# Performance work log

Hardware: AMD Instinct MI355X
Metric: run time of the kernel (lower is better)

The kernel has to match this reference:

```python
import jax, jax.numpy as jnp
import numpy as np

B, H = 1024, 256
HP = H // 2  # hyperparams_dim
W_SCALE = 0.08  # kaiming-uniform-like magnitude to keep tanh unsaturated


def setup_inputs() -> dict:
    key = jax.random.key(0)
    ks = jax.random.split(key, 8)
    return {
        "h_0": jax.random.normal(ks[0], (B, 1, H), dtype=jnp.float32),
        "h_t": jax.random.normal(ks[1], (B, 1, H), dtype=jnp.float32),
        "msg": jax.random.normal(ks[2], (B, 1, H), dtype=jnp.float32),
        "c": jax.random.uniform(ks[3], (1,), dtype=jnp.float32),
        "fc1_w": jax.random.normal(ks[4], (HP, H), dtype=jnp.float32) * W_SCALE,
        "fc2_w": jax.random.normal(ks[5], (HP, HP), dtype=jnp.float32) * W_SCALE,
        "fc3_w": jax.random.normal(ks[6], (HP, HP), dtype=jnp.float32) * W_SCALE,
        "fc4_w": jax.random.normal(ks[7], (2 * H * H, HP), dtype=jnp.float32) * W_SCALE,
    }


def reference(h_0, h_t, msg, c, fc1_w, fc2_w, fc3_w, fc4_w):
    # torch code clamps self.c into [0, 1] before use
    cc = jnp.clip(c, 0.0, 1.0)
    h = cc * h_0 + (1.0 - cc) * h_t                     # [B, 1, H]
    x = jnp.tanh(jnp.einsum('bsh,ph->bsp', h, fc1_w))    # [B, 1, HP]
    x = jnp.tanh(jnp.einsum('bsp,qp->bsq', x, fc2_w))    # [B, 1, HP]
    x = jnp.tanh(jnp.einsum('bsq,rq->bsr', x, fc3_w))    # [B, 1, HP]
    f4 = jnp.einsum('bsr,wr->bsw', x, fc4_w)             # [B, 1, 2*H*H]
    g1 = f4[..., : H * H].reshape(-1, H, H)              # [B, H, H]
    g2 = f4[..., H * H :].reshape(-1, H, H)              # [B, H, H]
    # F.linear(msg[i], g) == msg[i] @ g.T, batched over B
    g1_out = jnp.tanh(jnp.einsum('bsh,bkh->bsk', msg, g1))  # [B, 1, H]
    out = jnp.einsum('bsk,bok->bso', g1_out, g2)             # [B, 1, H]
    return out
```

## Files before the change

### kernel.cpp

```cpp
#include <hip/hip_runtime.h>
#include <hip/hip_bf16.h>

#define HDIM 256
#define HPDIM 128

typedef short bf8 __attribute__((ext_vector_type(8)));
typedef float f32x4 __attribute__((ext_vector_type(4)));

__device__ inline unsigned pkbf2(float a, float b) {
  float2 f; f.x = a; f.y = b;
  __hip_bfloat162 h = __float22bfloat162_rn(f);
  unsigned u; __builtin_memcpy(&u, &h, 4); return u;
}
__device__ inline unsigned short bfbits(float v) {
  __hip_bfloat16 h = __float2bfloat16(v);
  unsigned short u; __builtin_memcpy(&u, &h, 2); return u;
}
__device__ inline uint4 pack8u(float4 a, float4 b) {
  uint4 r;
  r.x = pkbf2(a.x, a.y); r.y = pkbf2(a.z, a.w);
  r.z = pkbf2(b.x, b.y); r.w = pkbf2(b.z, b.w);
  return r;
}
__device__ inline float fast_tanh(float x) {
  float t = __expf(2.0f * x);
  return 1.0f - 2.0f * __builtin_amdgcn_rcpf(t + 1.0f);
}
__device__ inline bf8 wfrag(const float* __restrict__ s) {
  float4 a = *(const float4*)s, b = *(const float4*)(s + 4);
  uint4 u = pack8u(a, b);
  bf8 r; __builtin_memcpy(&r, &u, 16); return r;
}

typedef const __attribute__((address_space(1))) unsigned int* gas_ptr;
typedef __attribute__((address_space(3))) unsigned int* las_ptr;
__device__ inline void gld_lds16(const void* g, void* l) {
  __builtin_amdgcn_global_load_lds((gas_ptr)g, (las_ptr)l, 16, 0, 0);
}

__global__ __launch_bounds__(256) void k_prep(
    const float* __restrict__ h0, const float* __restrict__ htv,
    const float* __restrict__ cp,
    const float* __restrict__ w1, const float* __restrict__ w2,
    const float* __restrict__ w3, const float* __restrict__ msg,
    short* __restrict__ x3f, float* __restrict__ msgTT) {
  const int t = threadIdx.x;
  const int bx = blockIdx.x;

  if (bx >= 64) {
    const int b0 = (bx - 64) * 64;
    #pragma unroll
    for (int it = 0; it < 16; ++it) {
      int u = it * 256 + t;
      int bl = u & 63, g = u >> 6;
      float4 v = *(const float4*)(msg + (size_t)(b0 + bl) * HDIM + g * 4);
      *(float4*)(msgTT + (size_t)g * 4096 + (b0 + bl) * 4) = v;
    }
    return;
  }

  __shared__ char hbuf[8192];
  __shared__ char xa[4096];
  __shared__ char xb[4096];
  const int wave = t >> 6, lane = t & 63;
  const int r16 = lane & 15, quad = lane >> 4;
  const int b0 = bx * 16;
  const float cc = fminf(fmaxf(cp[0], 0.f), 1.f);

  #pragma unroll
  for (int it = 0; it < 2; ++it) {
    int flat = it * 2048 + t * 8;
    int row = flat >> 8, col = flat & 255, kb = col >> 3;
    int gi = (b0 + row) * HDIM + col;
    float4 a = *(const float4*)(h0 + gi);
    float4 b = *(const float4*)(htv + gi);
    float4 va, vb;
    va.x = cc*a.x + (1.f-cc)*b.x; va.y = cc*a.y + (1.f-cc)*b.y;
    va.z = cc*a.z + (1.f-cc)*b.z; va.w = cc*a.w + (1.f-cc)*b.w;
    a = *(const float4*)(h0 + gi + 4); b = *(const float4*)(htv + gi + 4);
    vb.x = cc*a.x + (1.f-cc)*b.x; vb.y = cc*a.y + (1.f-cc)*b.y;
    vb.z = cc*a.z + (1.f-cc)*b.z; vb.w = cc*a.w + (1.f-cc)*b.w;
    *(uint4*)(hbuf + row*512 + ((kb ^ (row & 7)) << 4)) = pack8u(va, vb);
  }
  __syncthreads();

  {
    f32x4 acc[2] = {};
    #pragma unroll
    for (int ks = 0; ks < 8; ++ks) {
      bf8 af = *(bf8*)(hbuf + r16*512 + (((ks*4 + quad) ^ (r16 & 7)) << 4));
      #pragma unroll
      for (int nt = 0; nt < 2; ++nt) {
        bf8 bw_ = wfrag(w1 + ((wave*2 + nt)*16 + r16) * 256 + ks*32 + quad*8);
        acc[nt] = __builtin_amdgcn_mfma_f32_16x16x32_bf16(af, bw_, acc[nt], 0, 0, 0);
      }
    }
    #pragma unroll
    for (int nt = 0; nt < 2; ++nt)
      #pragma unroll
      for (int i = 0; i < 4; ++i) {
        int row = quad*4 + i, col = wave*32 + nt*16 + r16;
        *(unsigned short*)(xa + row*256 + (((col >> 3) ^ (row & 7)) << 4) + ((col & 7) << 1))
            = bfbits(fast_tanh(acc[nt][i]));
      }
  }
  __syncthreads();
  {
    f32x4 acc[2] = {};
    #pragma unroll
    for (int ks = 0; ks < 4; ++ks) {
      bf8 af = *(bf8*)(xa + r16*256 + (((ks*4 + quad) ^ (r16 & 7)) << 4));
      #pragma unroll
      for (int nt = 0; nt < 2; ++nt) {
        bf8 bw_ = wfrag(w2 + ((wave*2 + nt)*16 + r16) * 128 + ks*32 + quad*8);
        acc[nt] = __builtin_amdgcn_mfma_f32_16x16x32_bf16(af, bw_, acc[nt], 0, 0, 0);
      }
    }
    #pragma unroll
    for (int nt = 0; nt < 2; ++nt)
      #pragma unroll
      for (int i = 0; i < 4; ++i) {
        int row = quad*4 + i, col = wave*32 + nt*16 + r16;
        *(unsigned short*)(xb + row*256 + (((col >> 3) ^ (row & 7)) << 4) + ((col & 7) << 1))
            = bfbits(fast_tanh(acc[nt][i]));
      }
  }
  __syncthreads();
  {
    f32x4 acc[2] = {};
    #pragma unroll
    for (int ks = 0; ks < 4; ++ks) {
      bf8 af = *(bf8*)(xb + r16*256 + (((ks*4 + quad) ^ (r16 & 7)) << 4));
      #pragma unroll
      for (int nt = 0; nt < 2; ++nt) {
        bf8 bw_ = wfrag(w3 + ((wave*2 + nt)*16 + r16) * 128 + ks*32 + quad*8);
        acc[nt] = __builtin_amdgcn_mfma_f32_16x16x32_bf16(af, bw_, acc[nt], 0, 0, 0);
      }
    }
    #pragma unroll
    for (int nt = 0; nt < 2; ++nt)
      #pragma unroll
      for (int i = 0; i < 4; ++i) {
        int row = quad*4 + i, col = wave*32 + nt*16 + r16;
        *(unsigned short*)(xa + row*256 + (((col >> 3) ^ (row & 7)) << 4) + ((col & 7) << 1))
            = bfbits(fast_tanh(acc[nt][i]));
      }
  }
  __syncthreads();
  {
    int ks = t >> 6, l = t & 63, q2 = l >> 4, rr = l & 15;
    uint4 d = *(uint4*)(xa + rr*256 + (((ks*4 + q2) ^ (rr & 7)) << 4));
    *(uint4*)(x3f + (size_t)((bx*4 + ks)*64 + l)*8) = d;
  }
}

template<int PHASE>
__global__ __launch_bounds__(1024, 4) void k_hyper(
    const short* __restrict__ x3f, const float* __restrict__ wTT,
    const float* __restrict__ fc4, float* __restrict__ outp) {
  __shared__ char lds[65536 + 49152];
  char* slab = lds;
  char* ring = lds + 65536;
  const int bxs = blockIdx.x;
  const int kcol = ((bxs & 7) << 5) | (bxs >> 3);
  const int t = threadIdx.x, wave = t >> 6, lane = t & 63;
  const int r16 = lane & 15, quad = lane >> 4;
  const int bw = wave * 64;

  const float* src = fc4 + ((size_t)(PHASE ? 65536 : 0) + (size_t)kcol * 256) * HPDIM;

  gld_lds16(src + t * 4, ring + t * 16);

  bf8 xf[4][4];
  #pragma unroll
  for (int nt = 0; nt < 4; ++nt)
    #pragma unroll
    for (int ks = 0; ks < 4; ++ks)
      xf[nt][ks] = *(const bf8*)(x3f +
          (size_t)(((wave*4 + nt)*4 + ks)*64 + lane)*8);
  #pragma unroll
  for (int nt = 0; nt < 4; ++nt)
    #pragma unroll
    for (int ks = 0; ks < 4; ++ks)
      asm volatile("" : "+v"(xf[nt][ks]));

  #pragma unroll
  for (int c = 0; c < 8; ++c) {
    if (c < 7)
      gld_lds16(src + (c + 1) * 4096 + t * 4, ring + ((c + 1) % 3) * 16384 + t * 16);
    if (c < 7) asm volatile("s_waitcnt vmcnt(1) lgkmcnt(0)" ::: "memory");
    else       asm volatile("s_waitcnt vmcnt(0) lgkmcnt(0)" ::: "memory");
    __builtin_amdgcn_s_barrier();
    __builtin_amdgcn_sched_barrier(0);
    {
      f32x4 v = *(const f32x4*)(ring + (c % 3) * 16384 + t * 16);
      int row = c * 32 + (t >> 5), kb = (t & 31) >> 1;
      uint2 o; o.x = pkbf2(v[0], v[1]); o.y = pkbf2(v[2], v[3]);
      *(uint2*)(slab + row * 256 + ((kb ^ (row & 7)) << 4) + (t & 1) * 8) = o;
    }
  }
  __syncthreads();

  float gacc[4] = {0.f, 0.f, 0.f, 0.f};
  const float* wbase = wTT + (size_t)quad * 4096 + (bw + r16) * 4;

  #pragma unroll 1
  for (int hg = 0; hg < 16; ++hg) {
    float4 wv[4];
    #pragma unroll
    for (int nt = 0; nt < 4; ++nt)
      wv[nt] = *(const float4*)(wbase + (size_t)hg*16384 + nt*64);
    const int row = hg*16 + r16;
    bf8 af[4];
    #pragma unroll
    for (int ks = 0; ks < 4; ++ks)
      af[ks] = *(bf8*)(slab + row*256 + (((ks*4 + quad) ^ (row & 7)) << 4));
    #pragma unroll
    for (int nt = 0; nt < 4; ++nt) {
      f32x4 acc = {};
      #pragma unroll
      for (int ks = 0; ks < 4; ++ks)
        acc = __builtin_amdgcn_mfma_f32_16x16x32_bf16(af[ks], xf[nt][ks], acc, 0, 0, 0);
      gacc[nt] += acc[0]*wv[nt].x + acc[1]*wv[nt].y + acc[2]*wv[nt].z + acc[3]*wv[nt].w;
    }
  }

  #pragma unroll
  for (int nt = 0; nt < 4; ++nt) {
    float v = gacc[nt];
    v += __shfl_xor(v, 16);
    v += __shfl_xor(v, 32);
    if (quad == 0) {
      int b = bw + nt*16 + r16;
      if (PHASE == 0) outp[(size_t)(kcol >> 2)*4096 + b*4 + (kcol & 3)] = fast_tanh(v);
      else            outp[b*HDIM + kcol] = v;
    }
  }
}

extern "C" void kernel_launch(void* const* d_in, const int* in_sizes, int n_in,
                              void* d_out, int out_size, void* d_ws, size_t ws_size,
                              hipStream_t stream) {
  const float* h0  = (const float*)d_in[0];
  const float* htt = (const float*)d_in[1];
  const float* msg = (const float*)d_in[2];
  const float* c   = (const float*)d_in[3];
  const float* w1  = (const float*)d_in[4];
  const float* w2  = (const float*)d_in[5];
  const float* w3  = (const float*)d_in[6];
  const float* w4  = (const float*)d_in[7];
  float* out = (float*)d_out;

  short* x3f  = (short*)d_ws;
  float* g1TT = (float*)((char*)d_ws + 262144);
  float* msgTT= (float*)((char*)d_ws + 262144 + 1048576);

  k_prep<<<dim3(80), dim3(256), 0, stream>>>(h0, htt, c, w1, w2, w3, msg,
                                             x3f, msgTT);
  k_hyper<0><<<dim3(256), dim3(1024), 0, stream>>>(x3f, msgTT, w4, g1TT);
  k_hyper<1><<<dim3(256), dim3(1024), 0, stream>>>(x3f, g1TT, w4, out);
}
```

Measured before the change: 155.6 us.

## Overlap fc4 chunk streaming with MFMA compute using a double-buffered ring

New measurement: 215.2 us. 38.3% more time.

```diff
diff --git a/kernel.cpp b/kernel.cpp
--- a/kernel.cpp
+++ b/kernel.cpp
@@ -158,7 +158,7 @@
 __global__ __launch_bounds__(1024, 4) void k_hyper(
     const short* __restrict__ x3f, const float* __restrict__ wTT,
     const float* __restrict__ fc4, float* __restrict__ outp) {
-  __shared__ char lds[65536 + 49152];
+  __shared__ char lds[65536 + 32768];
   char* slab = lds;
   char* ring = lds + 65536;
   const int bxs = blockIdx.x;
@@ -184,44 +184,61 @@
     for (int ks = 0; ks < 4; ++ks)
       asm volatile("" : "+v"(xf[nt][ks]));
 
-  #pragma unroll
-  for (int c = 0; c < 8; ++c) {
-    if (c < 7)
-      gld_lds16(src + (c + 1) * 4096 + t * 4, ring + ((c + 1) % 3) * 16384 + t * 16);
-    if (c < 7) asm volatile("s_waitcnt vmcnt(1) lgkmcnt(0)" ::: "memory");
-    else       asm volatile("s_waitcnt vmcnt(0) lgkmcnt(0)" ::: "memory");
-    __builtin_amdgcn_s_barrier();
-    __builtin_amdgcn_sched_barrier(0);
-    {
-      f32x4 v = *(const f32x4*)(ring + (c % 3) * 16384 + t * 16);
-      int row = c * 32 + (t >> 5), kb = (t & 31) >> 1;
-      uint2 o; o.x = pkbf2(v[0], v[1]); o.y = pkbf2(v[2], v[3]);
-      *(uint2*)(slab + row * 256 + ((kb ^ (row & 7)) << 4) + (t & 1) * 8) = o;
-    }
-  }
-  __syncthreads();
+  asm volatile("s_waitcnt vmcnt(0) lgkmcnt(0)" ::: "memory");
+  __builtin_amdgcn_sched_barrier(0);
+  __builtin_amdgcn_s_barrier();
+  {
+    f32x4 v = *(const f32x4*)(ring + t * 16);
+    int row = t >> 5, kb = (t & 31) >> 1;
+    uint2 o; o.x = pkbf2(v[0], v[1]); o.y = pkbf2(v[2], v[3]);
+    *(uint2*)(slab + row * 256 + ((kb ^ (row & 7)) << 4) + (t & 1) * 8) = o;
+  }
+  gld_lds16(src + 4096 + t * 4, ring + 16384 + t * 16);
+  asm volatile("s_waitcnt lgkmcnt(0)" ::: "memory");
+  __builtin_amdgcn_sched_barrier(0);
+  __builtin_amdgcn_s_barrier();
 
   float gacc[4] = {0.f, 0.f, 0.f, 0.f};
   const float* wbase = wTT + (size_t)quad * 4096 + (bw + r16) * 4;
 
   #pragma unroll 1
-  for (int hg = 0; hg < 16; ++hg) {
-    float4 wv[4];
-    #pragma unroll
-    for (int nt = 0; nt < 4; ++nt)
-      wv[nt] = *(const float4*)(wbase + (size_t)hg*16384 + nt*64);
-    const int row = hg*16 + r16;
-    bf8 af[4];
-    #pragma unroll
-    for (int ks = 0; ks < 4; ++ks)
-      af[ks] = *(bf8*)(slab + row*256 + (((ks*4 + quad) ^ (row & 7)) << 4));
-    #pragma unroll
-    for (int nt = 0; nt < 4; ++nt) {
-      f32x4 acc = {};
+  for (int c = 0; c < 8; ++c) {
+    #pragma unroll
+    for (int hh = 0; hh < 2; ++hh) {
+      const int hg = c * 2 + hh;
+      float4 wv[4];
+      #pragma unroll
+      for (int nt = 0; nt < 4; ++nt)
+        wv[nt] = *(const float4*)(wbase + (size_t)hg*16384 + nt*64);
+      const int row = hg*16 + r16;
+      bf8 af[4];
       #pragma unroll
       for (int ks = 0; ks < 4; ++ks)
-        acc = __builtin_amdgcn_mfma_f32_16x16x32_bf16(af[ks], xf[nt][ks], acc, 0, 0, 0);
-      gacc[nt] += acc[0]*wv[nt].x + acc[1]*wv[nt].y + acc[2]*wv[nt].z + acc[3]*wv[nt].w;
+        af[ks] = *(bf8*)(slab + row*256 + (((ks*4 + quad) ^ (row & 7)) << 4));
+      #pragma unroll
+      for (int nt = 0; nt < 4; ++nt) {
+        f32x4 acc = {};
+        #pragma unroll
+        for (int ks = 0; ks < 4; ++ks)
+          acc = __builtin_amdgcn_mfma_f32_16x16x32_bf16(af[ks], xf[nt][ks], acc, 0, 0, 0);
+        gacc[nt] += acc[0]*wv[nt].x + acc[1]*wv[nt].y + acc[2]*wv[nt].z + acc[3]*wv[nt].w;
+      }
+    }
+    if (c < 7) {
+      asm volatile("s_waitcnt vmcnt(0)" ::: "memory");
+      __builtin_amdgcn_sched_barrier(0);
+      if (c + 2 < 8)
+        gld_lds16(src + (c + 2) * 4096 + t * 4, ring + ((c + 2) & 1) * 16384 + t * 16);
+      __builtin_amdgcn_s_barrier();
+      {
+        f32x4 v = *(const f32x4*)(ring + ((c + 1) & 1) * 16384 + t * 16);
+        int row = (c + 1) * 32 + (t >> 5), kb = (t & 31) >> 1;
+        uint2 o; o.x = pkbf2(v[0], v[1]); o.y = pkbf2(v[2], v[3]);
+        *(uint2*)(slab + row * 256 + ((kb ^ (row & 7)) << 4) + (t & 1) * 8) = o;
+      }
+      asm volatile("s_waitcnt lgkmcnt(0)" ::: "memory");
+      __builtin_amdgcn_sched_barrier(0);
+      __builtin_amdgcn_s_barrier();
     }
   }
 
```
